# Kernel tuning notes

Measured on AMD Instinct MI355X. Metric: run time of the kernel, lower is better.

The kernel has to match this reference:

```python
import jax, jax.numpy as jnp
import numpy as np

B, L, D, H = 4, 1024, 1024, 16
HS = D // H
BLOCK = 1024
EPS = 1e-5


def setup_inputs() -> dict:
    key = jax.random.key(0)
    ks = jax.random.split(key, 12)
    s = 0.02
    return {
        "x": jax.random.normal(ks[0], (B, L, D), jnp.float32),
        "ln1_w": jnp.ones((D,), jnp.float32),
        "ln1_b": jnp.zeros((D,), jnp.float32),
        "Wqkv": jax.random.normal(ks[1], (D, 3 * D), jnp.float32) * s,
        "bqkv": jnp.zeros((3 * D,), jnp.float32),
        "Wproj": jax.random.normal(ks[2], (D, D), jnp.float32) * s,
        "bproj": jnp.zeros((D,), jnp.float32),
        "Er": jax.random.normal(ks[3], (BLOCK, HS), jnp.float32) * s,
        "ln2_w": jnp.ones((D,), jnp.float32),
        "ln2_b": jnp.zeros((D,), jnp.float32),
        "Wfc": jax.random.normal(ks[4], (D, 4 * D), jnp.float32) * s,
        "bfc": jnp.zeros((4 * D,), jnp.float32),
        "Wfc2": jax.random.normal(ks[5], (4 * D, D), jnp.float32) * s,
        "bfc2": jnp.zeros((D,), jnp.float32),
    }


def _layernorm(x, w, b):
    mu = jnp.mean(x, axis=-1, keepdims=True)
    var = jnp.mean(jnp.square(x - mu), axis=-1, keepdims=True)
    return (x - mu) * jax.lax.rsqrt(var + EPS) * w + b


def _skew(QEr):
    # Music-Transformer skew: pad one zero column on the left of last dim,
    # reshape (B,H,L,L+1) -> (B,H,L+1,L), drop first row.
    b, h, l, _ = QEr.shape
    padded = jnp.pad(QEr, ((0, 0), (0, 0), (0, 0), (1, 0)))
    return padded.reshape(b, h, l + 1, l)[:, :, 1:, :]


def _block(x, ln1_w, ln1_b, Wqkv, bqkv, Wproj, bproj, Er,
           ln2_w, ln2_b, Wfc, bfc, Wfc2, bfc2):
    b, l, d = x.shape
    # --- attention on ln_1(x) ---
    h = _layernorm(x, ln1_w, ln1_b)
    qkv = h @ Wqkv + bqkv                      # (B, L, 3D)
    q, k, v = jnp.split(qkv, 3, axis=-1)
    q = q.reshape(b, l, H, HS).transpose(0, 2, 1, 3)  # (B,H,L,hs)
    k = k.reshape(b, l, H, HS).transpose(0, 2, 1, 3)
    v = v.reshape(b, l, H, HS).transpose(0, 2, 1, 3)

    start = BLOCK - l
    Er_t = Er[start:, :].T                     # (hs, L)
    QEr = jnp.einsum('bhld,dm->bhlm', q, Er_t)  # (B,H,L,L)
    Srel = _skew(QEr)

    QKt = jnp.einsum('bhld,bhmd->bhlm', q, k)  # (B,H,L,L)
    scale = 1.0 / jnp.sqrt(jnp.asarray(HS, x.dtype))
    att = (QKt + Srel) * scale
    causal = jnp.tril(jnp.ones((l, l), bool))
    att = jnp.where(causal, att, jnp.asarray(-jnp.inf, att.dtype))
    att = jax.nn.softmax(att, axis=-1)
    y = jnp.einsum('bhlm,bhmd->bhld', att, v)  # (B,H,L,hs)
    y = y.transpose(0, 2, 1, 3).reshape(b, l, d)
    a = y @ Wproj + bproj

    x = x + a
    # --- MLP on ln_2(x) ---
    h2 = _layernorm(x, ln2_w, ln2_b)
    m = jax.nn.gelu(h2 @ Wfc + bfc, approximate=False) @ Wfc2 + bfc2
    return x + m


def reference(x, ln1_w, ln1_b, Wqkv, bqkv, Wproj, bproj, Er,
              ln2_w, ln2_b, Wfc, bfc, Wfc2, bfc2):
    return _block(x, ln1_w, ln1_b, Wqkv, bqkv, Wproj, bproj, Er,
                  ln2_w, ln2_b, Wfc, bfc, Wfc2, bfc2)
```

## Files before the change

kernel.cpp:

```cpp
#include <hip/hip_runtime.h>
#include <hip/hip_bf16.h>
#include <math.h>

typedef __attribute__((ext_vector_type(8))) __bf16 bf16x8;
typedef __attribute__((ext_vector_type(4))) float f32x4;

#define LL 1024
#define DD 1024
#define HH 16

#define GLOAD16(g, l)                                              \
  __builtin_amdgcn_global_load_lds(                                \
      (const __attribute__((address_space(1))) void*)(g),          \
      (__attribute__((address_space(3))) void*)(l), 16, 0, 0)

#define FENCE asm volatile("" ::: "memory")
#define BARRIER do { FENCE; __builtin_amdgcn_s_barrier(); FENCE; } while (0)
#define SCHEDB __builtin_amdgcn_sched_barrier(0)

__global__ __launch_bounds__(256) void transpose_cvt(const float* __restrict__ W,
                                                     __hip_bfloat16* __restrict__ Wt,
                                                     int R, int C) {
  __shared__ float tile[32][33];
  int tx = threadIdx.x;
  int r0 = blockIdx.y * 32, c0 = blockIdx.x * 32;
  int r = tx >> 3, c4 = (tx & 7) * 4;
  float4 v = *(const float4*)&W[(size_t)(r0 + r) * C + c0 + c4];
  tile[r][c4 + 0] = v.x; tile[r][c4 + 1] = v.y;
  tile[r][c4 + 2] = v.z; tile[r][c4 + 3] = v.w;
  __syncthreads();
  int c = tx >> 3, r4 = (tx & 7) * 4;
  __hip_bfloat16 o[4];
#pragma unroll
  for (int j = 0; j < 4; ++j) o[j] = __float2bfloat16(tile[r4 + j][c]);
  *(uint2*)&Wt[(size_t)(c0 + c) * R + r0 + r4] = *(const uint2*)o;
}

__global__ __launch_bounds__(256) void cvt_er(const float* __restrict__ Er,
                                              __hip_bfloat16* __restrict__ Erb) {
  int i = blockIdx.x * 256 + threadIdx.x;
  float4 v = *(const float4*)&Er[(size_t)i * 4];
  __hip_bfloat16 o[4];
  o[0] = __float2bfloat16(v.x); o[1] = __float2bfloat16(v.y);
  o[2] = __float2bfloat16(v.z); o[3] = __float2bfloat16(v.w);
  *(uint2*)&Erb[(size_t)i * 4] = *(const uint2*)o;
}

__global__ __launch_bounds__(256) void ln_kernel(const float* __restrict__ X,
                                                 const float* __restrict__ w,
                                                 const float* __restrict__ b,
                                                 __hip_bfloat16* __restrict__ out) {
  int row = blockIdx.x;
  int tid = threadIdx.x;
  const float* xr = X + (size_t)row * DD;
  float4 v = *(const float4*)&xr[tid * 4];
  float s = v.x + v.y + v.z + v.w;
  float s2 = v.x * v.x + v.y * v.y + v.z * v.z + v.w * v.w;
#pragma unroll
  for (int m = 1; m < 64; m <<= 1) {
    s += __shfl_xor(s, m);
    s2 += __shfl_xor(s2, m);
  }
  __shared__ float ps[4], ps2[4];
  int wv_ = tid >> 6, lane = tid & 63;
  if (lane == 0) { ps[wv_] = s; ps2[wv_] = s2; }
  __syncthreads();
  float ts = ps[0] + ps[1] + ps[2] + ps[3];
  float ts2 = ps2[0] + ps2[1] + ps2[2] + ps2[3];
  float mu = ts * (1.0f / DD);
  float var = ts2 * (1.0f / DD) - mu * mu;
  float rs = rsqrtf(var + 1e-5f);
  float4 wv = *(const float4*)&w[tid * 4];
  float4 bv = *(const float4*)&b[tid * 4];
  __hip_bfloat16 o[4];
  o[0] = __float2bfloat16((v.x - mu) * rs * wv.x + bv.x);
  o[1] = __float2bfloat16((v.y - mu) * rs * wv.y + bv.y);
  o[2] = __float2bfloat16((v.z - mu) * rs * wv.z + bv.z);
  o[3] = __float2bfloat16((v.w - mu) * rs * wv.w + bv.w);
  *(uint2*)&out[(size_t)row * DD + tid * 4] = *(const uint2*)o;
}

template <int EPI>
__global__ __launch_bounds__(512) void gemm256(const __hip_bfloat16* __restrict__ A,
                                               const __hip_bfloat16* __restrict__ Bt,
                                               const float* __restrict__ bias,
                                               const float* __restrict__ resid,
                                               void* __restrict__ Cout,
                                               int M, int N, int K) {
  __shared__ __hip_bfloat16 Ab[4][256][32];
  __shared__ __hip_bfloat16 Bb[4][256][32];
  const int tid = threadIdx.x, lane = tid & 63, w = tid >> 6;
  const int wm = w >> 2, wn = w & 3;

  int nbx = gridDim.x, nwg = nbx * gridDim.y;
  int orig = blockIdx.y * nbx + blockIdx.x;
  int cpx = nwg >> 3;
  int wgid = (orig & 7) * cpx + (orig >> 3);
  int bm0 = (wgid / nbx) * 256, bn0 = (wgid % nbx) * 256;

  const int fr = lane & 15, kq = lane >> 4;
  const int sg = ((lane & 3) ^ ((lane >> 3) & 3)) * 8;
  const int srw = lane >> 2;

  auto stageA = [&](int c, int half, int k0) {
    const __hip_bfloat16* src =
        A + (size_t)(bm0 + half * 128 + w * 16 + srw) * K + k0 + sg;
    GLOAD16(src, (char*)Ab + c * 16384 + half * 8192 + w * 1024);
  };
  auto stageB = [&](int c, int half, int k0) {
    const __hip_bfloat16* src =
        Bt + (size_t)(bn0 + half * 128 + w * 16 + srw) * K + k0 + sg;
    GLOAD16(src, (char*)Bb + c * 16384 + half * 8192 + w * 1024);
  };
  const int swz = ((kq ^ ((fr >> 1) & 3)) << 4);
  auto ldA = [&](int c, int r) -> bf16x8 {
    return *(const bf16x8*)((const char*)Ab + c * 16384 + r * 64 + swz);
  };
  auto ldB = [&](int c, int r) -> bf16x8 {
    return *(const bf16x8*)((const char*)Bb + c * 16384 + r * 64 + swz);
  };

  f32x4 acc[8][4] = {};
  bf16x8 a[8], b0[2], b1[2];

  auto mm16 = [&](int no, bf16x8* br) {
    __builtin_amdgcn_s_setprio(1);
#pragma unroll
    for (int mf = 0; mf < 8; ++mf)
#pragma unroll
      for (int nf = 0; nf < 2; ++nf)
        acc[mf][no + nf] = __builtin_amdgcn_mfma_f32_16x16x32_bf16(
            a[mf], br[nf], acc[mf][no + nf], 0, 0, 0);
    __builtin_amdgcn_s_setprio(0);
  };

  const int nt = K >> 5;
#pragma unroll
  for (int tt = 0; tt < 3; ++tt) {
    stageA(tt, 0, tt * 32); stageA(tt, 1, tt * 32);
    stageB(tt, 0, tt * 32); stageB(tt, 1, tt * 32);
  }
  asm volatile("s_waitcnt vmcnt(8)" ::: "memory");
  BARRIER;

  for (int t = 0; t < nt; ++t) {
    const int cur = t & 3, nxt = (t + 3) & 3, kn = (t + 3) * 32;
    const bool st = (t + 3 < nt);
#pragma unroll
    for (int mf = 0; mf < 8; ++mf) a[mf] = ldA(cur, wm * 128 + mf * 16 + fr);
#pragma unroll
    for (int nf = 0; nf < 2; ++nf) b0[nf] = ldB(cur, wn * 64 + nf * 16 + fr);
    if (st) { stageA(nxt, 0, kn); stageA(nxt, 1, kn); }
    BARRIER; SCHEDB; mm16(0, b0); SCHEDB; BARRIER;
#pragma unroll
    for (int nf = 0; nf < 2; ++nf) b1[nf] = ldB(cur, wn * 64 + (nf + 2) * 16 + fr);
    if (st) { stageB(nxt, 0, kn); stageB(nxt, 1, kn); }
    BARRIER; SCHEDB; mm16(2, b1); SCHEDB;
    if (t <= nt - 4)      { asm volatile("s_waitcnt vmcnt(8)" ::: "memory"); }
    else if (t == nt - 3) { asm volatile("s_waitcnt vmcnt(4)" ::: "memory"); }
    else if (t == nt - 2) { asm volatile("s_waitcnt vmcnt(0)" ::: "memory"); }
    BARRIER;
  }

#pragma unroll
  for (int nf = 0; nf < 4; ++nf) {
    int col = bn0 + wn * 64 + nf * 16 + fr;
    float bsv = bias[col];
#pragma unroll
    for (int mf = 0; mf < 8; ++mf) {
      int rowb = bm0 + wm * 128 + mf * 16 + kq * 4;
#pragma unroll
      for (int j = 0; j < 4; ++j) {
        int row = rowb + j;
        float v = acc[mf][nf][j] + bsv;
        if (EPI == 1) v = 0.5f * v * (1.0f + erff(v * 0.7071067811865476f));
        if (EPI == 2) {
          ((float*)Cout)[(size_t)row * N + col] = v + resid[(size_t)row * N + col];
        } else {
          ((__hip_bfloat16*)Cout)[(size_t)row * N + col] = __float2bfloat16(v);
        }
      }
    }
  }
}

template <int EPI>
__global__ __launch_bounds__(256) void gemm128p(const __hip_bfloat16* __restrict__ A,
                                                const __hip_bfloat16* __restrict__ Bt,
                                                const float* __restrict__ bias,
                                                const float* __restrict__ resid,
                                                void* __restrict__ Cout,
                                                int M, int N, int K) {
  __shared__ __hip_bfloat16 Ab[5][128][32];
  __shared__ __hip_bfloat16 Bb[5][128][32];
  const int tid = threadIdx.x, lane = tid & 63, w = tid >> 6;
  const int wm = w >> 1, wn = w & 1;

  int nbx = gridDim.x, nwg = nbx * gridDim.y;
  int orig = blockIdx.y * nbx + blockIdx.x;
  int cpx = nwg >> 3;
  int wgid = (orig & 7) * cpx + (orig >> 3);
  int bm0 = (wgid / nbx) * 128, bn0 = (wgid % nbx) * 128;

  const int fr = lane & 15, kq = lane >> 4;
  const int sg = ((lane & 3) ^ ((lane >> 3) & 3)) * 8;
  const int srw = lane >> 2;

  auto stageA = [&](int c, int half, int k0) {
    const __hip_bfloat16* src =
        A + (size_t)(bm0 + half * 64 + w * 16 + srw) * K + k0 + sg;
    GLOAD16(src, (char*)Ab + c * 8192 + half * 4096 + w * 1024);
  };
  auto stageB = [&](int c, int half, int k0) {
    const __hip_bfloat16* src =
        Bt + (size_t)(bn0 + half * 64 + w * 16 + srw) * K + k0 + sg;
    GLOAD16(src, (char*)Bb + c * 8192 + half * 4096 + w * 1024);
  };
  const int swz = ((kq ^ ((fr >> 1) & 3)) << 4);
  auto ldA = [&](int c, int r) -> bf16x8 {
    return *(const bf16x8*)((const char*)Ab + c * 8192 + r * 64 + swz);
  };
  auto ldB = [&](int c, int r) -> bf16x8 {
    return *(const bf16x8*)((const char*)Bb + c * 8192 + r * 64 + swz);
  };

  f32x4 acc[4][4] = {};
  bf16x8 a[4], b[4];

  const int nt = K >> 5;
#pragma unroll
  for (int tt = 0; tt < 4; ++tt) {
    stageA(tt, 0, tt * 32); stageA(tt, 1, tt * 32);
    stageB(tt, 0, tt * 32); stageB(tt, 1, tt * 32);
  }
  asm volatile("s_waitcnt vmcnt(12)" ::: "memory");
  BARRIER;

  int cur = 0, nxt = 4;
  for (int t = 0; t < nt; ++t) {
    const int kn = (t + 4) * 32;
    const bool st = (t + 4 < nt);
#pragma unroll
    for (int mf = 0; mf < 4; ++mf) a[mf] = ldA(cur, wm * 64 + mf * 16 + fr);
#pragma unroll
    for (int nf = 0; nf < 4; ++nf) b[nf] = ldB(cur, wn * 64 + nf * 16 + fr);
    if (st) {
      stageA(nxt, 0, kn); stageA(nxt, 1, kn);
      stageB(nxt, 0, kn); stageB(nxt, 1, kn);
    }
    BARRIER; SCHEDB;
    __builtin_amdgcn_s_setprio(1);
#pragma unroll
    for (int mf = 0; mf < 4; ++mf)
#pragma unroll
      for (int nf = 0; nf < 4; ++nf)
        acc[mf][nf] = __builtin_amdgcn_mfma_f32_16x16x32_bf16(a[mf], b[nf], acc[mf][nf], 0, 0, 0);
    __builtin_amdgcn_s_setprio(0);
    SCHEDB;
    if (t <= nt - 5)      { asm volatile("s_waitcnt vmcnt(12)" ::: "memory"); }
    else if (t == nt - 4) { asm volatile("s_waitcnt vmcnt(8)" ::: "memory"); }
    else if (t == nt - 3) { asm volatile("s_waitcnt vmcnt(4)" ::: "memory"); }
    else if (t == nt - 2) { asm volatile("s_waitcnt vmcnt(0)" ::: "memory"); }
    BARRIER;
    cur = (cur == 4) ? 0 : cur + 1;
    nxt = (nxt == 4) ? 0 : nxt + 1;
  }

#pragma unroll
  for (int nf = 0; nf < 4; ++nf) {
    int col = bn0 + wn * 64 + nf * 16 + fr;
    float bsv = bias[col];
#pragma unroll
    for (int mf = 0; mf < 4; ++mf) {
      int rowb = bm0 + wm * 64 + mf * 16 + kq * 4;
#pragma unroll
      for (int j = 0; j < 4; ++j) {
        int row = rowb + j;
        float v = acc[mf][nf][j] + bsv;
        if (EPI == 1) v = 0.5f * v * (1.0f + erff(v * 0.7071067811865476f));
        if (EPI == 2) {
          ((float*)Cout)[(size_t)row * N + col] = v + resid[(size_t)row * N + col];
        } else {
          ((__hip_bfloat16*)Cout)[(size_t)row * N + col] = __float2bfloat16(v);
        }
      }
    }
  }
}

__global__ __launch_bounds__(256) void attn_mfma(const __hip_bfloat16* __restrict__ qkv,
                                                 const __hip_bfloat16* __restrict__ Erb,
                                                 __hip_bfloat16* __restrict__ Y) {
  __shared__ __hip_bfloat16 k_s[64][72];
  __shared__ __hip_bfloat16 er_s[128][72];
  __shared__ __hip_bfloat16 p_s[4][16][72];
  __shared__ __hip_bfloat16 g_s[4][16][128];
  __shared__ __hip_bfloat16 vt_s[64 * 64];

  int bid = blockIdx.x;
  int qi = 15 - (bid >> 6);
  int head = bid & 63;
  int h = head & 15, b = head >> 4;
  int l0 = qi * 64;
  int tid = threadIdx.x, lane = tid & 63, w = tid >> 6;
  const int fr = lane & 15, kq = lane >> 4;

  const __hip_bfloat16* base = qkv + (size_t)b * (LL * 3072) + h * 64;

  bf16x8 qf[2];
  {
    const __hip_bfloat16* q0 = base + (size_t)(l0 + 16 * w + fr) * 3072 + kq * 8;
    qf[0] = *(const bf16x8*)q0;
    qf[1] = *(const bf16x8*)(q0 + 32);
  }

  const int ksr = tid >> 2, ksd = (tid & 3) * 16;
  const __hip_bfloat16* ksrc = base + 1024 + (size_t)ksr * 3072 + ksd;
  const int vc = (tid >> 3) * 2, vd0 = (tid & 7) * 8;
  const __hip_bfloat16* vsrc = base + 2048 + (size_t)vc * 3072 + vd0;
  const int e0r = tid >> 1, e0c = (tid & 1) * 32;
  const int err = tid >> 2, erc = (tid & 3) * 16;

  uint4 kst0, kst1, vst0, vst1;
  uint4 est0, est1, est2, est3;
  uint4 ers0, ers1;

  {
    kst0 = *(const uint4*)ksrc; kst1 = *(const uint4*)(ksrc + 8);
    vst0 = *(const uint4*)vsrc; vst1 = *(const uint4*)(vsrc + 3072);
    int m = min(max(960 - l0 + e0r, 0), 1023);
    const __hip_bfloat16* ep = Erb + (size_t)m * 64 + e0c;
    est0 = *(const uint4*)ep;        est1 = *(const uint4*)(ep + 8);
    est2 = *(const uint4*)(ep + 16); est3 = *(const uint4*)(ep + 24);
  }

  f32x4 oacc[4] = {};
  float m_run[4], s_run[4];
#pragma unroll
  for (int j = 0; j < 4; ++j) { m_run[j] = -1e30f; s_run[j] = 0.f; }

  auto gchunk = [&](int hf) {
#pragma unroll
    for (int g = 0; g < 4; ++g) {
      int cc = hf * 64 + 16 * g + fr, kc = kq * 8;
      bf16x8 e0 = *(const bf16x8*)&er_s[cc][kc];
      bf16x8 e1 = *(const bf16x8*)&er_s[cc][kc + 32];
      f32x4 gacc = {};
      gacc = __builtin_amdgcn_mfma_f32_16x16x32_bf16(qf[0], e0, gacc, 0, 0, 0);
      gacc = __builtin_amdgcn_mfma_f32_16x16x32_bf16(qf[1], e1, gacc, 0, 0, 0);
#pragma unroll
      for (int j = 0; j < 4; ++j)
        g_s[w][kq * 4 + j][hf * 64 + 16 * g + fr] = __float2bfloat16(gacc[j]);
    }
  };

  for (int t = 0; t <= qi; ++t) {
    __syncthreads();
    *(uint4*)&k_s[ksr][ksd] = kst0;
    *(uint4*)&k_s[ksr][ksd + 8] = kst1;
    {
      const uint16_t* h0 = (const uint16_t*)&vst0;
      const uint16_t* h1 = (const uint16_t*)&vst1;
#pragma unroll
      for (int j = 0; j < 8; ++j) {
        int d = vd0 + j;
        uint32_t pk = (uint32_t)h0[j] | ((uint32_t)h1[j] << 16);
        uint32_t byte = ((uint32_t)d << 7) + 2u * (uint32_t)vc;
        byte ^= (uint32_t)(((d & 7) ^ (d >> 3)) << 4);
        *(uint32_t*)((char*)vt_s + byte) = pk;
      }
    }
    if (t == 0) {
      *(uint4*)&er_s[e0r][e0c]      = est0;
      *(uint4*)&er_s[e0r][e0c + 8]  = est1;
      *(uint4*)&er_s[e0r][e0c + 16] = est2;
      *(uint4*)&er_s[e0r][e0c + 24] = est3;
    } else if (t < qi) {
      int hf = (t + 1) & 1;
      *(uint4*)&er_s[hf * 64 + err][erc]     = ers0;
      *(uint4*)&er_s[hf * 64 + err][erc + 8] = ers1;
    }
    __syncthreads();
    if (t < qi) {
      int c0n = (t + 1) * 64;
      const __hip_bfloat16* kp = ksrc + (size_t)c0n * 3072;
      kst0 = *(const uint4*)kp; kst1 = *(const uint4*)(kp + 8);
      const __hip_bfloat16* vp = vsrc + (size_t)c0n * 3072;
      vst0 = *(const uint4*)vp; vst1 = *(const uint4*)(vp + 3072);
      if (t + 1 < qi) {
        int m = min(960 - l0 + (t + 2) * 64 + err, 1023);
        const __hip_bfloat16* ep = Erb + (size_t)m * 64 + erc;
        ers0 = *(const uint4*)ep; ers1 = *(const uint4*)(ep + 8);
      }
    }
    SCHEDB;

    f32x4 sacc[4] = {};
#pragma unroll
    for (int f = 0; f < 4; ++f) {
      int cc = 16 * f + fr, kc = kq * 8;
      bf16x8 k0 = *(const bf16x8*)&k_s[cc][kc];
      bf16x8 k1 = *(const bf16x8*)&k_s[cc][kc + 32];
      sacc[f] = __builtin_amdgcn_mfma_f32_16x16x32_bf16(qf[0], k0, sacc[f], 0, 0, 0);
      sacc[f] = __builtin_amdgcn_mfma_f32_16x16x32_bf16(qf[1], k1, sacc[f], 0, 0, 0);
    }
    if (t == 0) {
      gchunk(0);
      if (qi > 0) gchunk(1);
    } else if (t < qi) {
      gchunk((t + 1) & 1);
    }

    float sv[4][4];
#pragma unroll
    for (int f = 0; f < 4; ++f) {
#pragma unroll
      for (int j = 0; j < 4; ++j) {
        int r = kq * 4 + j;
        int c = 16 * f + fr;
        int jj = c - (16 * w + r) + 63;
        float g = __bfloat162float(g_s[w][r][(t * 64 + jj) & 127]);
        float val = (sacc[f][j] + g) * 0.125f;
        if (t == qi && c > 16 * w + r) val = -1e30f;
        sv[f][j] = val;
      }
    }
    float alpha[4];
#pragma unroll
    for (int j = 0; j < 4; ++j) {
      float tm = fmaxf(fmaxf(sv[0][j], sv[1][j]), fmaxf(sv[2][j], sv[3][j]));
      tm = fmaxf(tm, __shfl_xor(tm, 1));
      tm = fmaxf(tm, __shfl_xor(tm, 2));
      tm = fmaxf(tm, __shfl_xor(tm, 4));
      tm = fmaxf(tm, __shfl_xor(tm, 8));
      float nm = fmaxf(m_run[j], tm);
      alpha[j] = __expf(m_run[j] - nm);
      m_run[j] = nm;
    }
#pragma unroll
    for (int f = 0; f < 4; ++f)
#pragma unroll
      for (int j = 0; j < 4; ++j)
        sv[f][j] = __expf(sv[f][j] - m_run[j]);
#pragma unroll
    for (int j = 0; j < 4; ++j) {
      float ps = sv[0][j] + sv[1][j] + sv[2][j] + sv[3][j];
      ps += __shfl_xor(ps, 1); ps += __shfl_xor(ps, 2);
      ps += __shfl_xor(ps, 4); ps += __shfl_xor(ps, 8);
      s_run[j] = s_run[j] * alpha[j] + ps;
    }
#pragma unroll
    for (int f = 0; f < 4; ++f)
#pragma unroll
      for (int j = 0; j < 4; ++j)
        oacc[f][j] *= alpha[j];
#pragma unroll
    for (int f = 0; f < 4; ++f)
#pragma unroll
      for (int j = 0; j < 4; ++j)
        p_s[w][kq * 4 + j][16 * f + fr] = __float2bfloat16(sv[f][j]);
#pragma unroll
    for (int kk = 0; kk < 2; ++kk) {
      bf16x8 pf = *(const bf16x8*)&p_s[w][fr][kq * 8 + 32 * kk];
#pragma unroll
      for (int f = 0; f < 4; ++f) {
        int d = 16 * f + fr;
        int cc = kq * 8 + 32 * kk;
        uint32_t byte = ((uint32_t)d << 7) + 2u * (uint32_t)cc;
        byte ^= (uint32_t)(((d & 7) ^ (d >> 3)) << 4);
        bf16x8 vf = *(const bf16x8*)((char*)vt_s + byte);
        oacc[f] = __builtin_amdgcn_mfma_f32_16x16x32_bf16(pf, vf, oacc[f], 0, 0, 0);
      }
    }
  }

#pragma unroll
  for (int f = 0; f < 4; ++f)
#pragma unroll
    for (int j = 0; j < 4; ++j) {
      int r = 16 * w + kq * 4 + j;
      int d = 16 * f + fr;
      float o = oacc[f][j] / s_run[j];
      Y[(size_t)(b * LL + l0 + r) * DD + h * 64 + d] = __float2bfloat16(o);
    }
}

extern "C" void kernel_launch(void* const* d_in, const int* in_sizes, int n_in,
                              void* d_out, int out_size, void* d_ws, size_t ws_size,
                              hipStream_t stream) {
  (void)in_sizes; (void)n_in; (void)out_size; (void)ws_size;
  const float* x     = (const float*)d_in[0];
  const float* ln1w  = (const float*)d_in[1];
  const float* ln1b  = (const float*)d_in[2];
  const float* Wqkv  = (const float*)d_in[3];
  const float* bqkv  = (const float*)d_in[4];
  const float* Wproj = (const float*)d_in[5];
  const float* bproj = (const float*)d_in[6];
  const float* Er    = (const float*)d_in[7];
  const float* ln2w  = (const float*)d_in[8];
  const float* ln2b  = (const float*)d_in[9];
  const float* Wfc   = (const float*)d_in[10];
  const float* bfc   = (const float*)d_in[11];
  const float* Wfc2  = (const float*)d_in[12];
  const float* bfc2  = (const float*)d_in[13];
  float* out = (float*)d_out;

  char* ws = (char*)d_ws;
  const size_t MB = 1ull << 20;
  __hip_bfloat16* h1    = (__hip_bfloat16*)(ws + 0);
  __hip_bfloat16* qkvb  = (__hip_bfloat16*)(ws + 8 * MB);
  __hip_bfloat16* mbuf  = (__hip_bfloat16*)(ws + 0);
  __hip_bfloat16* yb    = (__hip_bfloat16*)(ws + 32 * MB);
  __hip_bfloat16* h2    = (__hip_bfloat16*)(ws + 32 * MB);
  float*          x2    = (float*)(ws + 40 * MB);
  __hip_bfloat16* Wqkvt = (__hip_bfloat16*)(ws + 56 * MB);
  __hip_bfloat16* Erb   = (__hip_bfloat16*)(ws + 62 * MB);
  __hip_bfloat16* Wprojt= (__hip_bfloat16*)(ws + 63 * MB);
  __hip_bfloat16* Wfct  = (__hip_bfloat16*)(ws + 66 * MB);
  __hip_bfloat16* Wfc2t = (__hip_bfloat16*)(ws + 75 * MB);

  dim3 blk(256);

  transpose_cvt<<<dim3(3072 / 32, 1024 / 32), blk, 0, stream>>>(Wqkv, Wqkvt, 1024, 3072);
  transpose_cvt<<<dim3(1024 / 32, 1024 / 32), blk, 0, stream>>>(Wproj, Wprojt, 1024, 1024);
  transpose_cvt<<<dim3(4096 / 32, 1024 / 32), blk, 0, stream>>>(Wfc, Wfct, 1024, 4096);
  transpose_cvt<<<dim3(1024 / 32, 4096 / 32), blk, 0, stream>>>(Wfc2, Wfc2t, 4096, 1024);
  cvt_er<<<dim3(64), blk, 0, stream>>>(Er, Erb);

  ln_kernel<<<4096, blk, 0, stream>>>(x, ln1w, ln1b, h1);

  gemm256<0><<<dim3(3072 / 256, 4096 / 256), dim3(512), 0, stream>>>(
      h1, Wqkvt, bqkv, nullptr, qkvb, 4096, 3072, 1024);

  attn_mfma<<<dim3(1024), blk, 0, stream>>>(qkvb, Erb, yb);

  gemm128p<2><<<dim3(1024 / 128, 4096 / 128), blk, 0, stream>>>(
      yb, Wprojt, bproj, x, x2, 4096, 1024, 1024);

  ln_kernel<<<4096, blk, 0, stream>>>(x2, ln2w, ln2b, h2);

  gemm256<1><<<dim3(4096 / 256, 4096 / 256), dim3(512), 0, stream>>>(
      h2, Wfct, bfc, nullptr, mbuf, 4096, 4096, 1024);

  gemm128p<2><<<dim3(1024 / 128, 4096 / 128), blk, 0, stream>>>(
      mbuf, Wfc2t, bfc2, x2, out, 4096, 1024, 4096);
}
```

Before: 255.5 us.

## Shrink QKV/FC GEMM tile to 256x128 with 3-stage pipeline

Replaces the 256x256 GEMM used for the QKV and FC1 projections with a 256x128 tile, triple-buffered LDS instead of quad-buffered, a simpler single-phase loop without the split MFMA halves and extra barriers, and launch bounds allowing more resident blocks. The aim is to double the grid (better CU fill on 256 CUs for 192/256-tile grids) and raise occupancy. In exchange each block has lower arithmetic intensity and more global/L2 traffic per FLOP, and the loop has fewer barriers for overlapping loads with MFMA.

```diff
diff --git a/kernel.cpp b/kernel.cpp
--- a/kernel.cpp
+++ b/kernel.cpp
@@ -81,85 +81,76 @@
 }
 
 template <int EPI>
-__global__ __launch_bounds__(512) void gemm256(const __hip_bfloat16* __restrict__ A,
-                                               const __hip_bfloat16* __restrict__ Bt,
-                                               const float* __restrict__ bias,
-                                               const float* __restrict__ resid,
-                                               void* __restrict__ Cout,
-                                               int M, int N, int K) {
-  __shared__ __hip_bfloat16 Ab[4][256][32];
-  __shared__ __hip_bfloat16 Bb[4][256][32];
+__global__ __launch_bounds__(512, 4) void gemm256x128(const __hip_bfloat16* __restrict__ A,
+                                                      const __hip_bfloat16* __restrict__ Bt,
+                                                      const float* __restrict__ bias,
+                                                      const float* __restrict__ resid,
+                                                      void* __restrict__ Cout,
+                                                      int M, int N, int K) {
+  __shared__ __hip_bfloat16 Ab[3][256][32];
+  __shared__ __hip_bfloat16 Bb[3][128][32];
   const int tid = threadIdx.x, lane = tid & 63, w = tid >> 6;
-  const int wm = w >> 2, wn = w & 3;
+  const int wm = w >> 1, wn = w & 1;
 
   int nbx = gridDim.x, nwg = nbx * gridDim.y;
   int orig = blockIdx.y * nbx + blockIdx.x;
   int cpx = nwg >> 3;
   int wgid = (orig & 7) * cpx + (orig >> 3);
-  int bm0 = (wgid / nbx) * 256, bn0 = (wgid % nbx) * 256;
+  int bm0 = (wgid / nbx) * 256, bn0 = (wgid % nbx) * 128;
 
   const int fr = lane & 15, kq = lane >> 4;
   const int sg = ((lane & 3) ^ ((lane >> 3) & 3)) * 8;
   const int srw = lane >> 2;
 
-  auto stageA = [&](int c, int half, int k0) {
-    const __hip_bfloat16* src =
-        A + (size_t)(bm0 + half * 128 + w * 16 + srw) * K + k0 + sg;
-    GLOAD16(src, (char*)Ab + c * 16384 + half * 8192 + w * 1024);
-  };
-  auto stageB = [&](int c, int half, int k0) {
-    const __hip_bfloat16* src =
-        Bt + (size_t)(bn0 + half * 128 + w * 16 + srw) * K + k0 + sg;
-    GLOAD16(src, (char*)Bb + c * 16384 + half * 8192 + w * 1024);
+  auto stageA = [&](int c, int g, int k0) {
+    int u = w * 2 + g;
+    const __hip_bfloat16* src = A + (size_t)(bm0 + u * 16 + srw) * K + k0 + sg;
+    GLOAD16(src, (char*)Ab + c * 16384 + u * 1024);
+  };
+  auto stageB = [&](int c, int k0) {
+    const __hip_bfloat16* src = Bt + (size_t)(bn0 + w * 16 + srw) * K + k0 + sg;
+    GLOAD16(src, (char*)Bb + c * 8192 + w * 1024);
   };
   const int swz = ((kq ^ ((fr >> 1) & 3)) << 4);
   auto ldA = [&](int c, int r) -> bf16x8 {
     return *(const bf16x8*)((const char*)Ab + c * 16384 + r * 64 + swz);
   };
   auto ldB = [&](int c, int r) -> bf16x8 {
-    return *(const bf16x8*)((const char*)Bb + c * 16384 + r * 64 + swz);
-  };
-
-  f32x4 acc[8][4] = {};
-  bf16x8 a[8], b0[2], b1[2];
-
-  auto mm16 = [&](int no, bf16x8* br) {
+    return *(const bf16x8*)((const char*)Bb + c * 8192 + r * 64 + swz);
+  };
+
+  f32x4 acc[4][4] = {};
+  bf16x8 a[4], b[4];
+
+  const int nt = K >> 5;
+#pragma unroll
+  for (int tt = 0; tt < 2; ++tt) {
+    stageA(tt, 0, tt * 32); stageA(tt, 1, tt * 32); stageB(tt, tt * 32);
+  }
+  asm volatile("s_waitcnt vmcnt(3)" ::: "memory");
+  BARRIER;
+
+  int cur = 0, nxt = 2;
+  for (int t = 0; t < nt; ++t) {
+#pragma unroll
+    for (int mf = 0; mf < 4; ++mf) a[mf] = ldA(cur, wm * 64 + mf * 16 + fr);
+#pragma unroll
+    for (int nf = 0; nf < 4; ++nf) b[nf] = ldB(cur, wn * 64 + nf * 16 + fr);
+    if (t + 2 < nt) {
+      stageA(nxt, 0, (t + 2) * 32); stageA(nxt, 1, (t + 2) * 32); stageB(nxt, (t + 2) * 32);
+    }
     __builtin_amdgcn_s_setprio(1);
 #pragma unroll
-    for (int mf = 0; mf < 8; ++mf)
-#pragma unroll
-      for (int nf = 0; nf < 2; ++nf)
-        acc[mf][no + nf] = __builtin_amdgcn_mfma_f32_16x16x32_bf16(
-            a[mf], br[nf], acc[mf][no + nf], 0, 0, 0);
+    for (int mf = 0; mf < 4; ++mf)
+#pragma unroll
+      for (int nf = 0; nf < 4; ++nf)
+        acc[mf][nf] = __builtin_amdgcn_mfma_f32_16x16x32_bf16(a[mf], b[nf], acc[mf][nf], 0, 0, 0);
     __builtin_amdgcn_s_setprio(0);
-  };
-
-  const int nt = K >> 5;
-#pragma unroll
-  for (int tt = 0; tt < 3; ++tt) {
-    stageA(tt, 0, tt * 32); stageA(tt, 1, tt * 32);
-    stageB(tt, 0, tt * 32); stageB(tt, 1, tt * 32);
-  }
-  asm volatile("s_waitcnt vmcnt(8)" ::: "memory");
-  BARRIER;
-
-  for (int t = 0; t < nt; ++t) {
-    const int cur = t & 3, nxt = (t + 3) & 3, kn = (t + 3) * 32;
-    const bool st = (t + 3 < nt);
-#pragma unroll
-    for (int mf = 0; mf < 8; ++mf) a[mf] = ldA(cur, wm * 128 + mf * 16 + fr);
-#pragma unroll
-    for (int nf = 0; nf < 2; ++nf) b0[nf] = ldB(cur, wn * 64 + nf * 16 + fr);
-    if (st) { stageA(nxt, 0, kn); stageA(nxt, 1, kn); }
-    BARRIER; SCHEDB; mm16(0, b0); SCHEDB; BARRIER;
-#pragma unroll
-    for (int nf = 0; nf < 2; ++nf) b1[nf] = ldB(cur, wn * 64 + (nf + 2) * 16 + fr);
-    if (st) { stageB(nxt, 0, kn); stageB(nxt, 1, kn); }
-    BARRIER; SCHEDB; mm16(2, b1); SCHEDB;
-    if (t <= nt - 4)      { asm volatile("s_waitcnt vmcnt(8)" ::: "memory"); }
-    else if (t == nt - 3) { asm volatile("s_waitcnt vmcnt(4)" ::: "memory"); }
+    if (t <= nt - 3)      { asm volatile("s_waitcnt vmcnt(3)" ::: "memory"); }
     else if (t == nt - 2) { asm volatile("s_waitcnt vmcnt(0)" ::: "memory"); }
     BARRIER;
+    cur = (cur == 2) ? 0 : cur + 1;
+    nxt = (nxt == 2) ? 0 : nxt + 1;
   }
 
 #pragma unroll
@@ -167,8 +158,8 @@
     int col = bn0 + wn * 64 + nf * 16 + fr;
     float bsv = bias[col];
 #pragma unroll
-    for (int mf = 0; mf < 8; ++mf) {
-      int rowb = bm0 + wm * 128 + mf * 16 + kq * 4;
+    for (int mf = 0; mf < 4; ++mf) {
+      int rowb = bm0 + wm * 64 + mf * 16 + kq * 4;
 #pragma unroll
       for (int j = 0; j < 4; ++j) {
         int row = rowb + j;
@@ -529,7 +520,7 @@
 
   ln_kernel<<<4096, blk, 0, stream>>>(x, ln1w, ln1b, h1);
 
-  gemm256<0><<<dim3(3072 / 256, 4096 / 256), dim3(512), 0, stream>>>(
+  gemm256x128<0><<<dim3(3072 / 128, 4096 / 256), dim3(512), 0, stream>>>(
       h1, Wqkvt, bqkv, nullptr, qkvb, 4096, 3072, 1024);
 
   attn_mfma<<<dim3(1024), blk, 0, stream>>>(qkvb, Erb, yb);
@@ -539,7 +530,7 @@
 
   ln_kernel<<<4096, blk, 0, stream>>>(x2, ln2w, ln2b, h2);
 
-  gemm256<1><<<dim3(4096 / 256, 4096 / 256), dim3(512), 0, stream>>>(
+  gemm256x128<1><<<dim3(4096 / 128, 4096 / 256), dim3(512), 0, stream>>>(
       h2, Wfct, bfc, nullptr, mbuf, 4096, 4096, 1024);
 
   gemm128p<2><<<dim3(1024 / 128, 4096 / 128), blk, 0, stream>>>(
```

Result: no change. 255.9 us (+0.2%).
